# Optimization experiments

Hardware: AMD Instinct MI355X
Metric: run time of the kernel (lower is better)

## Reference

```python
import jax, jax.numpy as jnp
import numpy as np

N, E, M, F, L = 50000, 800000, 50000, 64, 20
HID = 32
NEG_SLOPE = 0.2


def gatv2(x, src, dst, Wl, Wr, att, b, heads, outc):
    # PyG GATv2Conv (eval mode, dropout off), self-loops already in src/dst.
    n = x.shape[0]
    xl = (x @ Wl).reshape(n, heads, outc)
    xr = (x @ Wr).reshape(n, heads, outc)
    e = jax.nn.leaky_relu(xl[src] + xr[dst], NEG_SLOPE)          # [E, H, C]
    score = jnp.einsum('ehc,hc->eh', e, att)                      # [E, H]
    smax = jax.ops.segment_max(score, dst, num_segments=n)
    ex = jnp.exp(score - smax[dst])
    denom = jax.ops.segment_sum(ex, dst, num_segments=n)
    alpha = ex / denom[dst]                                       # scatter-softmax
    out = jax.ops.segment_sum(alpha[:, :, None] * xl[src], dst, num_segments=n)
    return out.reshape(n, heads * outc) + b


def setup_inputs() -> dict:
    key = jax.random.key(0)
    ks = jax.random.split(key, 32)
    d = {}
    d['x'] = jax.random.normal(ks[0], (N, 60), jnp.float32)
    d['lane_x'] = jax.random.normal(ks[1], (M, 2), jnp.float32)
    d['centerline'] = jax.random.normal(ks[2], (F, L, 2), jnp.float32)
    d['edge_index'] = jax.random.randint(ks[3], (2, E), 0, N)
    d['focal_idx'] = jax.random.randint(ks[4], (F,), 0, N)
    s = 0.1
    d['emb_W'] = jax.random.normal(ks[5], (60, HID)) * s
    d['emb_b'] = jnp.zeros((HID,))
    d['c1_Wl'] = jax.random.normal(ks[6], (HID, 4 * HID)) * s
    d['c1_Wr'] = jax.random.normal(ks[7], (HID, 4 * HID)) * s
    d['c1_att'] = jax.random.normal(ks[8], (4, HID)) * s
    d['c1_b'] = jnp.zeros((4 * HID,))
    d['c2_Wl'] = jax.random.normal(ks[9], (4 * HID, 4 * HID)) * s
    d['c2_Wr'] = jax.random.normal(ks[10], (4 * HID, 4 * HID)) * s
    d['c2_att'] = jax.random.normal(ks[11], (4, HID)) * s
    d['c2_b'] = jnp.zeros((4 * HID,))
    d['map_W'] = jax.random.normal(ks[12], (2, HID)) * s
    d['map_b'] = jnp.zeros((HID,))
    d['gg_Wl'] = jax.random.normal(ks[13], (4 * HID, HID)) * s
    d['gg_Wr'] = jax.random.normal(ks[14], (4 * HID, HID)) * s
    d['gg_att'] = jax.random.normal(ks[15], (1, HID)) * s
    d['gg_b'] = jnp.zeros((HID,))
    d['cl_W'] = jax.random.normal(ks[16], (2, HID)) * s
    d['cl_b'] = jnp.zeros((HID,))
    d['fc1_W'] = jax.random.normal(ks[17], (3 * HID, HID)) * s
    d['fc1_b'] = jnp.zeros((HID,))
    d['fc2_W'] = jax.random.normal(ks[18], (HID, HID // 2)) * s
    d['fc2_b'] = jnp.zeros((HID // 2,))
    d['fco_W'] = jax.random.normal(ks[19], (HID // 2, 60)) * s
    d['fco_b'] = jnp.zeros((60,))
    return d


def reference(x, lane_x, centerline, edge_index, focal_idx,
              emb_W, emb_b, c1_Wl, c1_Wr, c1_att, c1_b,
              c2_Wl, c2_Wr, c2_att, c2_b, map_W, map_b,
              gg_Wl, gg_Wr, gg_att, gg_b, cl_W, cl_b,
              fc1_W, fc1_b, fc2_W, fc2_b, fco_W, fco_b):
    n = x.shape[0]
    loops = jnp.arange(n)
    src = jnp.concatenate([edge_index[0], loops])  # PyG adds self-loops
    dst = jnp.concatenate([edge_index[1], loops])
    # agent encoder + subgraph (two GATv2 layers, heads=4, concat)
    h = jax.nn.relu(x @ emb_W + emb_b)                                   # [N,32]
    h = jax.nn.relu(gatv2(h, src, dst, c1_Wl, c1_Wr, c1_att, c1_b, 4, HID))
    agent_feat = jax.nn.relu(gatv2(h, src, dst, c2_Wl, c2_Wr, c2_att, c2_b, 4, HID))  # [N,128]
    # map branch (executable path: no lane edges -> plain embedding + mean pool)
    map_x = jax.nn.relu(lane_x @ map_W + map_b)                          # [M,32]
    map_global = jnp.mean(map_x, axis=0, keepdims=True)                  # [1,32]
    # global graph (heads=1)
    gf = jax.nn.relu(gatv2(agent_feat, src, dst, gg_Wl, gg_Wr, gg_att, gg_b, 1, HID))  # [N,32]
    focal = gf[focal_idx]                                                # [F,32]
    map_g = jnp.broadcast_to(map_global, (focal.shape[0], HID))
    cl = jnp.mean(centerline, axis=1) @ cl_W + cl_b                      # [F,32]
    comb = jnp.concatenate([focal, map_g, cl], axis=1)                   # [F,96]
    h = jax.nn.relu(comb @ fc1_W + fc1_b)
    h = jax.nn.relu(h @ fc2_W + fc2_b)
    return h @ fco_W + fco_b                                             # [F,60]
```

## Files before the change

kernel.cpp:

```cpp
#include <hip/hip_runtime.h>
#include <hip/hip_bf16.h>
#include <hip/hip_fp16.h>

typedef _Float16 half_t;
typedef _Float16 h8 __attribute__((ext_vector_type(8)));
typedef _Float16 h4v __attribute__((ext_vector_type(4)));
typedef _Float16 h2v __attribute__((ext_vector_type(2)));
typedef float f4v __attribute__((ext_vector_type(4)));

static inline int cdiv(long a, long b) { return (int)((a + b - 1) / b); }

__device__ __forceinline__ void fma4(float4& a, float s, const float4& w) {
    a.x += s * w.x; a.y += s * w.y; a.z += s * w.z; a.w += s * w.w;
}


template <int K4, int C4, int R>
__global__ __launch_bounds__(256) void gemm_t_h(
        const float* __restrict__ X, const float* __restrict__ W,
        const float* __restrict__ bias, half_t* __restrict__ Y,
        int Nr, int relu) {
    int idx = blockIdx.x * blockDim.x + threadIdx.x;
    int total = (Nr / R) * C4;
    if (idx >= total) return;
    int c4 = idx % C4;
    int n0 = (idx / C4) * R;
    const float4* __restrict__ Wv = (const float4*)W;
    const float4* __restrict__ Xv = (const float4*)X;
    float4 acc[R];
    float4 binit = bias ? ((const float4*)bias)[c4] : make_float4(0.f, 0.f, 0.f, 0.f);
#pragma unroll
    for (int r = 0; r < R; ++r) acc[r] = binit;
#pragma unroll 4
    for (int k4 = 0; k4 < K4; ++k4) {
        float4 w0 = Wv[(size_t)(4 * k4 + 0) * C4 + c4];
        float4 w1 = Wv[(size_t)(4 * k4 + 1) * C4 + c4];
        float4 w2 = Wv[(size_t)(4 * k4 + 2) * C4 + c4];
        float4 w3 = Wv[(size_t)(4 * k4 + 3) * C4 + c4];
#pragma unroll
        for (int r = 0; r < R; ++r) {
            float4 xv = Xv[(size_t)(n0 + r) * K4 + k4];
            fma4(acc[r], xv.x, w0); fma4(acc[r], xv.y, w1);
            fma4(acc[r], xv.z, w2); fma4(acc[r], xv.w, w3);
        }
    }
#pragma unroll
    for (int r = 0; r < R; ++r) {
        float4 o = acc[r];
        if (relu) {
            o.x = fmaxf(o.x, 0.f); o.y = fmaxf(o.y, 0.f);
            o.z = fmaxf(o.z, 0.f); o.w = fmaxf(o.w, 0.f);
        }
        h4v oh; oh.x = (half_t)o.x; oh.y = (half_t)o.y; oh.z = (half_t)o.z; oh.w = (half_t)o.w;
        ((h4v*)Y)[(size_t)(n0 + r) * C4 + c4] = oh;
    }
}


__global__ void wtrans(const float* __restrict__ c1l, const float* __restrict__ c1r,
                       const float* __restrict__ c2l, const float* __restrict__ c2r,
                       const float* __restrict__ ggl, const float* __restrict__ ggr,
                       half_t* __restrict__ dst) {
    int idx = blockIdx.x * blockDim.x + threadIdx.x;
    if (idx >= 49152) return;
    const float* src; int K, C, loc;
    if (idx < 8192) {
        K = 32; C = 128;
        if (idx < 4096) { src = c1l; loc = idx; } else { src = c1r; loc = idx - 4096; }
    } else if (idx < 40960) {
        K = 128; C = 128;
        if (idx < 24576) { src = c2l; loc = idx - 8192; } else { src = c2r; loc = idx - 24576; }
    } else {
        K = 128; C = 32;
        if (idx < 45056) { src = ggl; loc = idx - 40960; } else { src = ggr; loc = idx - 45056; }
    }
    int k = loc % K, c = loc / K;
    dst[idx] = (half_t)src[k * C + c];
}


template <int K, int C1>
__global__ __launch_bounds__(256) void mfma_dual(
        const half_t* __restrict__ Xh,
        const half_t* __restrict__ W1t, const half_t* __restrict__ W2t,
        half_t* __restrict__ Y1, half_t* __restrict__ Y2, int Nr) {
    constexpr int KT = K / 32;
    constexpr int NBC = (2 * C1) / 64;
    int wave = threadIdx.x >> 6, lane = threadIdx.x & 63;
    int bCol = blockIdx.x % NBC;
    int bRow = blockIdx.x / NBC;
    int rowBase = bRow * 128 + wave * 32;
    int colBase = bCol * 64;
    int m = lane & 15, quad = lane >> 4;

    f4v acc[2][4] = {};

    const half_t* bptr[4];
#pragma unroll
    for (int nt = 0; nt < 4; ++nt) {
        int gc = colBase + nt * 16 + m;
        bptr[nt] = (gc < C1) ? (W1t + (size_t)gc * K) : (W2t + (size_t)(gc - C1) * K);
    }
    int r0 = rowBase + m, r1 = rowBase + 16 + m;
    int r0c = (r0 < Nr) ? r0 : (Nr - 1);
    int r1c = (r1 < Nr) ? r1 : (Nr - 1);
    const half_t* a0p = Xh + (size_t)r0c * K + quad * 8;
    const half_t* a1p = Xh + (size_t)r1c * K + quad * 8;

#pragma unroll
    for (int kk = 0; kk < KT; ++kk) {
        h8 a0 = *(const h8*)(a0p + kk * 32);
        h8 a1 = *(const h8*)(a1p + kk * 32);
#pragma unroll
        for (int nt = 0; nt < 4; ++nt) {
            h8 b = *(const h8*)(bptr[nt] + kk * 32 + quad * 8);
            acc[0][nt] = __builtin_amdgcn_mfma_f32_16x16x32_f16(a0, b, acc[0][nt], 0, 0, 0);
            acc[1][nt] = __builtin_amdgcn_mfma_f32_16x16x32_f16(a1, b, acc[1][nt], 0, 0, 0);
        }
    }

#pragma unroll
    for (int mt = 0; mt < 2; ++mt) {
#pragma unroll
        for (int nt = 0; nt < 4; ++nt) {
            int gc = colBase + nt * 16 + m;
            half_t* Y = (gc < C1) ? (Y1 + gc) : (Y2 + (gc - C1));
#pragma unroll
            for (int r = 0; r < 4; ++r) {
                int gr = rowBase + mt * 16 + quad * 4 + r;
                if (gr < Nr) Y[(size_t)gr * C1] = (half_t)acc[mt][nt][r];
            }
        }
    }
}


__global__ void count_dst(const int* __restrict__ ei, int* __restrict__ counts,
                          int E, int Etot) {
    int e = blockIdx.x * blockDim.x + threadIdx.x;
    if (e >= Etot) return;
    int d = (e < E) ? ei[E + e] : (e - E);
    atomicAdd(&counts[d], 1);
}

#define SCAN_CH 2048

__global__ void reduce_chunks(const int* __restrict__ counts, int* __restrict__ partial, int N) {
    __shared__ int sh[256];
    int t = threadIdx.x, base = blockIdx.x * SCAN_CH + t * 8;
    int s = 0;
    for (int j = 0; j < 8; ++j) if (base + j < N) s += counts[base + j];
    sh[t] = s; __syncthreads();
    for (int off = 128; off >= 1; off >>= 1) {
        if (t < off) sh[t] += sh[t + off];
        __syncthreads();
    }
    if (t == 0) partial[blockIdx.x] = sh[0];
}

__global__ void scan_partials(int* __restrict__ partial, int nch) {
    if (threadIdx.x == 0 && blockIdx.x == 0) {
        int run = 0;
        for (int i = 0; i < nch; ++i) { int v = partial[i]; partial[i] = run; run += v; }
    }
}

__global__ void scan_chunks(const int* __restrict__ counts, const int* __restrict__ partial,
                            int* __restrict__ offsets, int N) {
    __shared__ int sh[256];
    int t = threadIdx.x, b = blockIdx.x, base = b * SCAN_CH + t * 8;
    int v[8], s = 0;
    for (int j = 0; j < 8; ++j) { v[j] = (base + j < N) ? counts[base + j] : 0; s += v[j]; }
    sh[t] = s; __syncthreads();
    for (int off = 1; off < 256; off <<= 1) {
        int x = (t >= off) ? sh[t - off] : 0;
        __syncthreads();
        sh[t] += x;
        __syncthreads();
    }
    int run = partial[b] + (t == 0 ? 0 : sh[t - 1]);
    for (int j = 0; j < 8; ++j) {
        if (base + j < N) offsets[base + j] = run;
        run += v[j];
    }
}

__global__ void fill_adj(const int* __restrict__ ei, const int* __restrict__ offsets,
                         int* __restrict__ cursor, int* __restrict__ adj, int E, int Etot) {
    int e = blockIdx.x * blockDim.x + threadIdx.x;
    if (e >= Etot) return;
    int s, d;
    if (e < E) { s = ei[e]; d = ei[E + e]; } else { s = e - E; d = s; }
    int pos = offsets[d] + atomicAdd(&cursor[d], 1);
    adj[pos] = s;
}


__device__ __forceinline__ float score16h(float x0, float y0, float xrx, float xry, float2 at) {
    float vx = x0 + xrx; vx = (vx > 0.f) ? vx : 0.2f * vx;
    float vy = y0 + xry; vy = (vy > 0.f) ? vy : 0.2f * vy;
    float p = vx * at.x + vy * at.y;
    p += __shfl_xor(p, 1); p += __shfl_xor(p, 2);
    p += __shfl_xor(p, 4); p += __shfl_xor(p, 8);
    return p;
}

__global__ __launch_bounds__(256) void gat_fused_h4_h(
        const half_t* __restrict__ xl, const half_t* __restrict__ xr,
        const float* __restrict__ att, const int* __restrict__ offsets,
        const int* __restrict__ counts, const int* __restrict__ adj,
        const float* __restrict__ bias, half_t* __restrict__ out, int N) {
    int wave = threadIdx.x >> 6, lane = threadIdx.x & 63;
    int d = blockIdx.x * 4 + wave;
    if (d >= N) return;
    int c = lane * 2;
    float2 at = *(const float2*)(att + c);
    h2v xrh = *(const h2v*)(xr + (long)d * 128 + c);
    float xrx = (float)xrh.x, xry = (float)xrh.y;
    int off = offsets[d], deg = counts[d];
    float lsum = 0.f, ax = 0.f, ay = 0.f;
    int i = 0;
    for (; i + 4 <= deg; i += 4) {
        int s0 = adj[off + i + 0], s1 = adj[off + i + 1];
        int s2 = adj[off + i + 2], s3 = adj[off + i + 3];
        h2v h0 = *(const h2v*)(xl + (long)s0 * 128 + c);
        h2v h1 = *(const h2v*)(xl + (long)s1 * 128 + c);
        h2v h2 = *(const h2v*)(xl + (long)s2 * 128 + c);
        h2v h3 = *(const h2v*)(xl + (long)s3 * 128 + c);
        float x0 = (float)h0.x, y0 = (float)h0.y;
        float x1 = (float)h1.x, y1 = (float)h1.y;
        float x2 = (float)h2.x, y2 = (float)h2.y;
        float x3 = (float)h3.x, y3 = (float)h3.y;
        float p0 = score16h(x0, y0, xrx, xry, at);
        float p1 = score16h(x1, y1, xrx, xry, at);
        float p2 = score16h(x2, y2, xrx, xry, at);
        float p3 = score16h(x3, y3, xrx, xry, at);
        float w0 = __expf(p0), w1 = __expf(p1), w2 = __expf(p2), w3 = __expf(p3);
        ax += w0 * x0 + w1 * x1 + w2 * x2 + w3 * x3;
        ay += w0 * y0 + w1 * y1 + w2 * y2 + w3 * y3;
        lsum += (w0 + w1) + (w2 + w3);
    }
    for (; i < deg; ++i) {
        int s = adj[off + i];
        h2v h0 = *(const h2v*)(xl + (long)s * 128 + c);
        float x0 = (float)h0.x, y0 = (float)h0.y;
        float w = __expf(score16h(x0, y0, xrx, xry, at));
        ax += w * x0; ay += w * y0; lsum += w;
    }
    float2 bb = *(const float2*)(bias + c);
    float inv = 1.f / lsum;
    h2v o;
    o.x = (half_t)fmaxf(ax * inv + bb.x, 0.f);
    o.y = (half_t)fmaxf(ay * inv + bb.y, 0.f);
    *(h2v*)(out + (long)d * 128 + c) = o;
}

__device__ __forceinline__ float score32h(float v0, float xr1, float at) {
    float v = v0 + xr1; v = (v > 0.f) ? v : 0.2f * v;
    float p = v * at;
    p += __shfl_xor(p, 1); p += __shfl_xor(p, 2); p += __shfl_xor(p, 4);
    p += __shfl_xor(p, 8); p += __shfl_xor(p, 16);
    return p;
}

__global__ __launch_bounds__(256) void gat_fused_h1_h(
        const half_t* __restrict__ xl, const half_t* __restrict__ xr,
        const float* __restrict__ att, const int* __restrict__ offsets,
        const int* __restrict__ counts, const int* __restrict__ adj,
        const float* __restrict__ bias, float* __restrict__ out, int N) {
    int sub = threadIdx.x >> 5, lane = threadIdx.x & 31;
    int d = blockIdx.x * 8 + sub;
    if (d >= N) return;
    float at = att[lane];
    float xr1 = (float)xr[(long)d * 32 + lane];
    int off = offsets[d], deg = counts[d];
    float lsum = 0.f, acc = 0.f;
    int i = 0;
    for (; i + 4 <= deg; i += 4) {
        int s0 = adj[off + i + 0], s1 = adj[off + i + 1];
        int s2 = adj[off + i + 2], s3 = adj[off + i + 3];
        float x0 = (float)xl[(long)s0 * 32 + lane];
        float x1 = (float)xl[(long)s1 * 32 + lane];
        float x2 = (float)xl[(long)s2 * 32 + lane];
        float x3 = (float)xl[(long)s3 * 32 + lane];
        float w0 = __expf(score32h(x0, xr1, at));
        float w1 = __expf(score32h(x1, xr1, at));
        float w2 = __expf(score32h(x2, xr1, at));
        float w3 = __expf(score32h(x3, xr1, at));
        acc += w0 * x0 + w1 * x1 + w2 * x2 + w3 * x3;
        lsum += (w0 + w1) + (w2 + w3);
    }
    for (; i < deg; ++i) {
        int s = adj[off + i];
        float x0 = (float)xl[(long)s * 32 + lane];
        float w = __expf(score32h(x0, xr1, at));
        acc += w * x0; lsum += w;
    }
    out[(long)d * 32 + lane] = fmaxf(acc / lsum + bias[lane], 0.f);
}


__global__ void map_sum_kernel(const float* __restrict__ lane_x, const float* __restrict__ map_W,
                               const float* __restrict__ map_b, float* __restrict__ sums, int M) {
    __shared__ float s[32];
    if (threadIdx.x < 32) s[threadIdx.x] = 0.f;
    __syncthreads();
    int t = blockIdx.x * blockDim.x + threadIdx.x;
    int nth = gridDim.x * blockDim.x;
    int c = t & 31;
    float w0 = map_W[c], w1 = map_W[32 + c], bb = map_b[c];
    float acc = 0.f;
    for (int m = t >> 5; m < M; m += nth >> 5) {
        float v = lane_x[(long)m * 2] * w0 + lane_x[(long)m * 2 + 1] * w1 + bb;
        acc += fmaxf(v, 0.f);
    }
    atomicAdd(&s[c], acc);
    __syncthreads();
    if (threadIdx.x < 32) atomicAdd(&sums[threadIdx.x], s[threadIdx.x]);
}


__global__ void head_kernel(const float* __restrict__ gf, const int* __restrict__ focal_idx,
                            const float* __restrict__ map_sums, int M,
                            const float* __restrict__ centerline, int L,
                            const float* __restrict__ cl_W, const float* __restrict__ cl_b,
                            const float* __restrict__ fc1_W, const float* __restrict__ fc1_b,
                            const float* __restrict__ fc2_W, const float* __restrict__ fc2_b,
                            const float* __restrict__ fco_W, const float* __restrict__ fco_b,
                            float* __restrict__ out) {
    int f = blockIdx.x;
    int lane = threadIdx.x;
    __shared__ float s_comb[96];
    __shared__ float s_h1[32];
    __shared__ float s_h2[16];
    __shared__ float s_cl[2];

    float c0 = 0.f, c1 = 0.f;
    if (lane < L) {
        c0 = centerline[((long)f * L + lane) * 2 + 0];
        c1 = centerline[((long)f * L + lane) * 2 + 1];
    }
    for (int off = 32; off >= 1; off >>= 1) {
        c0 += __shfl_down(c0, off);
        c1 += __shfl_down(c1, off);
    }
    if (lane == 0) { s_cl[0] = c0 / (float)L; s_cl[1] = c1 / (float)L; }
    __syncthreads();

    int fi = focal_idx[f];
    if (lane < 32) {
        s_comb[lane] = gf[(long)fi * 32 + lane];
        s_comb[32 + lane] = map_sums[lane] / (float)M;
        s_comb[64 + lane] = s_cl[0] * cl_W[lane] + s_cl[1] * cl_W[32 + lane] + cl_b[lane];
    }
    __syncthreads();

    if (lane < 32) {
        float acc = fc1_b[lane];
        for (int k = 0; k < 96; ++k) acc += s_comb[k] * fc1_W[k * 32 + lane];
        s_h1[lane] = fmaxf(acc, 0.f);
    }
    __syncthreads();

    if (lane < 16) {
        float acc = fc2_b[lane];
        for (int k = 0; k < 32; ++k) acc += s_h1[k] * fc2_W[k * 16 + lane];
        s_h2[lane] = fmaxf(acc, 0.f);
    }
    __syncthreads();

    if (lane < 60) {
        float acc = fco_b[lane];
        for (int k = 0; k < 16; ++k) acc += s_h2[k] * fco_W[k * 60 + lane];
        out[(long)f * 60 + lane] = acc;
    }
}


extern "C" void kernel_launch(void* const* d_in, const int* in_sizes, int n_in,
                              void* d_out, int out_size, void* d_ws, size_t ws_size,
                              hipStream_t stream) {
    const float* x          = (const float*)d_in[0];
    const float* lane_x     = (const float*)d_in[1];
    const float* centerline = (const float*)d_in[2];
    const int*   ei         = (const int*)d_in[3];
    const int*   focal_idx  = (const int*)d_in[4];
    const float* emb_W = (const float*)d_in[5];
    const float* emb_b = (const float*)d_in[6];
    const float* c1_Wl = (const float*)d_in[7];
    const float* c1_Wr = (const float*)d_in[8];
    const float* c1_att = (const float*)d_in[9];
    const float* c1_b  = (const float*)d_in[10];
    const float* c2_Wl = (const float*)d_in[11];
    const float* c2_Wr = (const float*)d_in[12];
    const float* c2_att = (const float*)d_in[13];
    const float* c2_b  = (const float*)d_in[14];
    const float* map_W = (const float*)d_in[15];
    const float* map_b = (const float*)d_in[16];
    const float* gg_Wl = (const float*)d_in[17];
    const float* gg_Wr = (const float*)d_in[18];
    const float* gg_att = (const float*)d_in[19];
    const float* gg_b  = (const float*)d_in[20];
    const float* cl_W  = (const float*)d_in[21];
    const float* cl_b  = (const float*)d_in[22];
    const float* fc1_W = (const float*)d_in[23];
    const float* fc1_b = (const float*)d_in[24];
    const float* fc2_W = (const float*)d_in[25];
    const float* fc2_b = (const float*)d_in[26];
    const float* fco_W = (const float*)d_in[27];
    const float* fco_b = (const float*)d_in[28];

    const int N = in_sizes[0] / 60;
    const int M = in_sizes[1] / 2;
    const int F = in_sizes[4];
    const int L = in_sizes[2] / (F * 2);
    const int E = in_sizes[3] / 2;
    const int Etot = E + N;

    half_t* Xl_h = (half_t*)d_ws;
    half_t* Xr_h = Xl_h + (size_t)N * 128;
    half_t* H0_h = Xr_h + (size_t)N * 128;
    half_t* H1_h = H0_h + (size_t)N * 32;
    half_t* AF_h = H1_h + (size_t)N * 128;
    float*  GF_f = (float*)(AF_h + (size_t)N * 128);
    half_t* Wt   = (half_t*)(GF_f + (size_t)N * 32);
    int* counts  = (int*)(Wt + 49152);
    int* offsets = counts + N;
    int* cursor  = offsets + N;
    int* adj     = cursor + N;
    float* MAPS  = (float*)(adj + Etot);
    int* partial = (int*)(MAPS + 32);

    half_t* c1Wlt = Wt + 0;
    half_t* c1Wrt = Wt + 4096;
    half_t* c2Wlt = Wt + 8192;
    half_t* c2Wrt = Wt + 24576;
    half_t* ggWlt = Wt + 40960;
    half_t* ggWrt = Wt + 45056;

    const int BS = 256;
    const int nch = cdiv(N, SCAN_CH);
    const int rowBlocks = cdiv(N, 128);

    hipMemsetAsync(counts, 0, (size_t)N * sizeof(int), stream);
    hipMemsetAsync(cursor, 0, (size_t)N * sizeof(int), stream);
    count_dst<<<cdiv(Etot, BS), BS, 0, stream>>>(ei, counts, E, Etot);
    reduce_chunks<<<nch, 256, 0, stream>>>(counts, partial, N);
    scan_partials<<<1, 64, 0, stream>>>(partial, nch);
    scan_chunks<<<nch, 256, 0, stream>>>(counts, partial, offsets, N);
    fill_adj<<<cdiv(Etot, BS), BS, 0, stream>>>(ei, offsets, cursor, adj, E, Etot);

    wtrans<<<cdiv(49152, BS), BS, 0, stream>>>(c1_Wl, c1_Wr, c2_Wl, c2_Wr, gg_Wl, gg_Wr, Wt);

    gemm_t_h<15, 8, 4><<<cdiv((long)(N / 4) * 8, BS), BS, 0, stream>>>(x, emb_W, emb_b, H0_h, N, 1);

    mfma_dual<32, 128><<<rowBlocks * 4, 256, 0, stream>>>(H0_h, c1Wlt, c1Wrt, Xl_h, Xr_h, N);
    gat_fused_h4_h<<<cdiv(N, 4), 256, 0, stream>>>(Xl_h, Xr_h, c1_att, offsets, counts, adj, c1_b, H1_h, N);

    mfma_dual<128, 128><<<rowBlocks * 4, 256, 0, stream>>>(H1_h, c2Wlt, c2Wrt, Xl_h, Xr_h, N);
    gat_fused_h4_h<<<cdiv(N, 4), 256, 0, stream>>>(Xl_h, Xr_h, c2_att, offsets, counts, adj, c2_b, AF_h, N);

    mfma_dual<128, 32><<<rowBlocks * 1, 256, 0, stream>>>(AF_h, ggWlt, ggWrt, Xl_h, Xr_h, N);
    gat_fused_h1_h<<<cdiv(N, 8), 256, 0, stream>>>(Xl_h, Xr_h, gg_att, offsets, counts, adj, gg_b, GF_f, N);

    hipMemsetAsync(MAPS, 0, 32 * sizeof(float), stream);
    map_sum_kernel<<<64, BS, 0, stream>>>(lane_x, map_W, map_b, MAPS, M);

    head_kernel<<<F, 64, 0, stream>>>(GF_f, focal_idx, MAPS, M, centerline, L,
                                      cl_W, cl_b, fc1_W, fc1_b, fc2_W, fc2_b,
                                      fco_W, fco_b, (float*)d_out);
}
```

Before: 439.2 us.

## Map eight destinations per wave in GAT aggregation with packed fp16 scoring

Rewrites the GATv2 aggregation kernels so each wave handles eight destination nodes with eight lanes each. Each lane loads 16 contiguous fp16 features per neighbor as wide vectors, computes leaky-relu and the attention dot product in packed fp16 (fdot2), and reduces per head with a single shuffle. The aim is to cut shuffle-reduction overhead and raise memory-level parallelism compared with one destination per wave. The cost is that lanes in a wave loop up to the max degree among their eight nodes, leaving some lanes idle. Scores are also now computed in fp16, which loses precision, and the attention vectors are converted to fp16 in the weight-transpose kernel.

```diff
diff --git a/kernel.cpp b/kernel.cpp
--- a/kernel.cpp
+++ b/kernel.cpp
@@ -8,10 +8,42 @@
 typedef _Float16 h2v __attribute__((ext_vector_type(2)));
 typedef float f4v __attribute__((ext_vector_type(4)));
 
+union H8u { h8 v; h2v h2[4]; _Float16 e[8]; };
+union H4u { h4v v; h2v h2[2]; _Float16 e[4]; };
+
 static inline int cdiv(long a, long b) { return (int)((a + b - 1) / b); }
 
 __device__ __forceinline__ void fma4(float4& a, float s, const float4& w) {
     a.x += s * w.x; a.y += s * w.y; a.z += s * w.z; a.w += s * w.w;
+}
+
+__device__ __forceinline__ h8 hmax8(h8 a, h8 b) {
+#if __has_builtin(__builtin_elementwise_max)
+    return __builtin_elementwise_max(a, b);
+#else
+    h8 r;
+#pragma unroll
+    for (int j = 0; j < 8; ++j) r[j] = (a[j] > b[j]) ? a[j] : b[j];
+    return r;
+#endif
+}
+__device__ __forceinline__ h4v hmax4(h4v a, h4v b) {
+#if __has_builtin(__builtin_elementwise_max)
+    return __builtin_elementwise_max(a, b);
+#else
+    h4v r;
+#pragma unroll
+    for (int j = 0; j < 4; ++j) r[j] = (a[j] > b[j]) ? a[j] : b[j];
+    return r;
+#endif
+}
+
+__device__ __forceinline__ float dot2acc(h2v a, h2v b, float c) {
+#if __has_builtin(__builtin_amdgcn_fdot2)
+    return __builtin_amdgcn_fdot2(a, b, c, false);
+#else
+    return c + (float)a.x * (float)b.x + (float)a.y * (float)b.y;
+#endif
 }
 
 
@@ -60,22 +92,33 @@
 __global__ void wtrans(const float* __restrict__ c1l, const float* __restrict__ c1r,
                        const float* __restrict__ c2l, const float* __restrict__ c2r,
                        const float* __restrict__ ggl, const float* __restrict__ ggr,
-                       half_t* __restrict__ dst) {
+                       const float* __restrict__ at1, const float* __restrict__ at2,
+                       const float* __restrict__ atg, half_t* __restrict__ dst) {
     int idx = blockIdx.x * blockDim.x + threadIdx.x;
-    if (idx >= 49152) return;
-    const float* src; int K, C, loc;
+    if (idx >= 49440) return;
+    if (idx >= 49152) {
+        int j = idx - 49152;
+        float v = (j < 128) ? at1[j] : (j < 256) ? at2[j - 128] : atg[j - 256];
+        dst[idx] = (half_t)v;
+        return;
+    }
+    const float* src; int K, loc;
     if (idx < 8192) {
-        K = 32; C = 128;
+        K = 32;
         if (idx < 4096) { src = c1l; loc = idx; } else { src = c1r; loc = idx - 4096; }
+        int k = loc % K, c = loc / K;
+        dst[idx] = (half_t)src[k * 128 + c];
     } else if (idx < 40960) {
-        K = 128; C = 128;
+        K = 128;
         if (idx < 24576) { src = c2l; loc = idx - 8192; } else { src = c2r; loc = idx - 24576; }
+        int k = loc % K, c = loc / K;
+        dst[idx] = (half_t)src[k * 128 + c];
     } else {
-        K = 128; C = 32;
+        K = 128;
         if (idx < 45056) { src = ggl; loc = idx - 40960; } else { src = ggr; loc = idx - 45056; }
-    }
-    int k = loc % K, c = loc / K;
-    dst[idx] = (half_t)src[k * C + c];
+        int k = loc % K, c = loc / K;
+        dst[idx] = (half_t)src[k * 32 + c];
+    }
 }
 
 
@@ -196,107 +239,129 @@
 }
 
 
-__device__ __forceinline__ float score16h(float x0, float y0, float xrx, float xry, float2 at) {
-    float vx = x0 + xrx; vx = (vx > 0.f) ? vx : 0.2f * vx;
-    float vy = y0 + xry; vy = (vy > 0.f) ? vy : 0.2f * vy;
-    float p = vx * at.x + vy * at.y;
-    p += __shfl_xor(p, 1); p += __shfl_xor(p, 2);
-    p += __shfl_xor(p, 4); p += __shfl_xor(p, 8);
-    return p;
-}
-
-__global__ __launch_bounds__(256) void gat_fused_h4_h(
+__global__ __launch_bounds__(256) void gat8_h4(
         const half_t* __restrict__ xl, const half_t* __restrict__ xr,
-        const float* __restrict__ att, const int* __restrict__ offsets,
+        const half_t* __restrict__ atth, const int* __restrict__ offsets,
         const int* __restrict__ counts, const int* __restrict__ adj,
         const float* __restrict__ bias, half_t* __restrict__ out, int N) {
     int wave = threadIdx.x >> 6, lane = threadIdx.x & 63;
-    int d = blockIdx.x * 4 + wave;
-    if (d >= N) return;
-    int c = lane * 2;
-    float2 at = *(const float2*)(att + c);
-    h2v xrh = *(const h2v*)(xr + (long)d * 128 + c);
-    float xrx = (float)xrh.x, xry = (float)xrh.y;
-    int off = offsets[d], deg = counts[d];
-    float lsum = 0.f, ax = 0.f, ay = 0.f;
-    int i = 0;
-    for (; i + 4 <= deg; i += 4) {
-        int s0 = adj[off + i + 0], s1 = adj[off + i + 1];
-        int s2 = adj[off + i + 2], s3 = adj[off + i + 3];
-        h2v h0 = *(const h2v*)(xl + (long)s0 * 128 + c);
-        h2v h1 = *(const h2v*)(xl + (long)s1 * 128 + c);
-        h2v h2 = *(const h2v*)(xl + (long)s2 * 128 + c);
-        h2v h3 = *(const h2v*)(xl + (long)s3 * 128 + c);
-        float x0 = (float)h0.x, y0 = (float)h0.y;
-        float x1 = (float)h1.x, y1 = (float)h1.y;
-        float x2 = (float)h2.x, y2 = (float)h2.y;
-        float x3 = (float)h3.x, y3 = (float)h3.y;
-        float p0 = score16h(x0, y0, xrx, xry, at);
-        float p1 = score16h(x1, y1, xrx, xry, at);
-        float p2 = score16h(x2, y2, xrx, xry, at);
-        float p3 = score16h(x3, y3, xrx, xry, at);
-        float w0 = __expf(p0), w1 = __expf(p1), w2 = __expf(p2), w3 = __expf(p3);
-        ax += w0 * x0 + w1 * x1 + w2 * x2 + w3 * x3;
-        ay += w0 * y0 + w1 * y1 + w2 * y2 + w3 * y3;
-        lsum += (w0 + w1) + (w2 + w3);
-    }
-    for (; i < deg; ++i) {
-        int s = adj[off + i];
-        h2v h0 = *(const h2v*)(xl + (long)s * 128 + c);
-        float x0 = (float)h0.x, y0 = (float)h0.y;
-        float w = __expf(score16h(x0, y0, xrx, xry, at));
-        ax += w * x0; ay += w * y0; lsum += w;
-    }
-    float2 bb = *(const float2*)(bias + c);
-    float inv = 1.f / lsum;
-    h2v o;
-    o.x = (half_t)fmaxf(ax * inv + bb.x, 0.f);
-    o.y = (half_t)fmaxf(ay * inv + bb.y, 0.f);
-    *(h2v*)(out + (long)d * 128 + c) = o;
-}
-
-__device__ __forceinline__ float score32h(float v0, float xr1, float at) {
-    float v = v0 + xr1; v = (v > 0.f) ? v : 0.2f * v;
-    float p = v * at;
-    p += __shfl_xor(p, 1); p += __shfl_xor(p, 2); p += __shfl_xor(p, 4);
-    p += __shfl_xor(p, 8); p += __shfl_xor(p, 16);
-    return p;
-}
-
-__global__ __launch_bounds__(256) void gat_fused_h1_h(
+    int g = lane >> 3, t = lane & 7;
+    int d = blockIdx.x * 32 + wave * 8 + g;
+    int dc = (d < N) ? d : (N - 1);
+    int off = offsets[dc];
+    int deg = (d < N) ? counts[dc] : 0;
+    int dmax = deg;
+    dmax = max(dmax, __shfl_xor(dmax, 8));
+    dmax = max(dmax, __shfl_xor(dmax, 16));
+    dmax = max(dmax, __shfl_xor(dmax, 32));
+
+    const half_t* xrp = xr + (size_t)dc * 128 + t * 16;
+    h8 xr_lo = *(const h8*)(xrp);
+    h8 xr_hi = *(const h8*)(xrp + 8);
+    H8u at_lo, at_hi;
+    at_lo.v = *(const h8*)(atth + t * 16);
+    at_hi.v = *(const h8*)(atth + t * 16 + 8);
+
+    float acc[16];
+#pragma unroll
+    for (int j = 0; j < 16; ++j) acc[j] = 0.f;
+    float lsum = 0.f;
+    h8 c02;
+#pragma unroll
+    for (int j = 0; j < 8; ++j) c02[j] = (half_t)0.2f;
+
+    for (int i = 0; i < dmax; ++i) {
+        bool valid = (i < deg);
+        int s = adj[off + (valid ? i : 0)];
+        const half_t* xp = xl + (size_t)s * 128 + t * 16;
+        H8u a_lo, a_hi;
+        a_lo.v = *(const h8*)(xp);
+        a_hi.v = *(const h8*)(xp + 8);
+        h8 v_lo = a_lo.v + xr_lo;
+        h8 v_hi = a_hi.v + xr_hi;
+        H8u lk_lo, lk_hi;
+        lk_lo.v = hmax8(v_lo, v_lo * c02);
+        lk_hi.v = hmax8(v_hi, v_hi * c02);
+        float p = 0.f;
+#pragma unroll
+        for (int j = 0; j < 4; ++j) p = dot2acc(lk_lo.h2[j], at_lo.h2[j], p);
+#pragma unroll
+        for (int j = 0; j < 4; ++j) p = dot2acc(lk_hi.h2[j], at_hi.h2[j], p);
+        p += __shfl_xor(p, 1);
+        float w = valid ? __expf(p) : 0.f;
+        lsum += w;
+#pragma unroll
+        for (int j = 0; j < 8; ++j) acc[j] += w * (float)a_lo.e[j];
+#pragma unroll
+        for (int j = 0; j < 8; ++j) acc[8 + j] += w * (float)a_hi.e[j];
+    }
+
+    if (d < N) {
+        float inv = 1.f / lsum;
+        H8u o_lo, o_hi;
+#pragma unroll
+        for (int j = 0; j < 8; ++j)
+            o_lo.e[j] = (half_t)fmaxf(acc[j] * inv + bias[t * 16 + j], 0.f);
+#pragma unroll
+        for (int j = 0; j < 8; ++j)
+            o_hi.e[j] = (half_t)fmaxf(acc[8 + j] * inv + bias[t * 16 + 8 + j], 0.f);
+        half_t* op = out + (size_t)d * 128 + t * 16;
+        *(h8*)(op) = o_lo.v;
+        *(h8*)(op + 8) = o_hi.v;
+    }
+}
+
+__global__ __launch_bounds__(256) void gat8_h1(
         const half_t* __restrict__ xl, const half_t* __restrict__ xr,
-        const float* __restrict__ att, const int* __restrict__ offsets,
+        const half_t* __restrict__ atth, const int* __restrict__ offsets,
         const int* __restrict__ counts, const int* __restrict__ adj,
         const float* __restrict__ bias, float* __restrict__ out, int N) {
-    int sub = threadIdx.x >> 5, lane = threadIdx.x & 31;
-    int d = blockIdx.x * 8 + sub;
-    if (d >= N) return;
-    float at = att[lane];
-    float xr1 = (float)xr[(long)d * 32 + lane];
-    int off = offsets[d], deg = counts[d];
-    float lsum = 0.f, acc = 0.f;
-    int i = 0;
-    for (; i + 4 <= deg; i += 4) {
-        int s0 = adj[off + i + 0], s1 = adj[off + i + 1];
-        int s2 = adj[off + i + 2], s3 = adj[off + i + 3];
-        float x0 = (float)xl[(long)s0 * 32 + lane];
-        float x1 = (float)xl[(long)s1 * 32 + lane];
-        float x2 = (float)xl[(long)s2 * 32 + lane];
-        float x3 = (float)xl[(long)s3 * 32 + lane];
-        float w0 = __expf(score32h(x0, xr1, at));
-        float w1 = __expf(score32h(x1, xr1, at));
-        float w2 = __expf(score32h(x2, xr1, at));
-        float w3 = __expf(score32h(x3, xr1, at));
-        acc += w0 * x0 + w1 * x1 + w2 * x2 + w3 * x3;
-        lsum += (w0 + w1) + (w2 + w3);
-    }
-    for (; i < deg; ++i) {
-        int s = adj[off + i];
-        float x0 = (float)xl[(long)s * 32 + lane];
-        float w = __expf(score32h(x0, xr1, at));
-        acc += w * x0; lsum += w;
-    }
-    out[(long)d * 32 + lane] = fmaxf(acc / lsum + bias[lane], 0.f);
+    int wave = threadIdx.x >> 6, lane = threadIdx.x & 63;
+    int g = lane >> 3, t = lane & 7;
+    int d = blockIdx.x * 32 + wave * 8 + g;
+    int dc = (d < N) ? d : (N - 1);
+    int off = offsets[dc];
+    int deg = (d < N) ? counts[dc] : 0;
+    int dmax = deg;
+    dmax = max(dmax, __shfl_xor(dmax, 8));
+    dmax = max(dmax, __shfl_xor(dmax, 16));
+    dmax = max(dmax, __shfl_xor(dmax, 32));
+
+    h4v xr4 = *(const h4v*)(xr + (size_t)dc * 32 + t * 4);
+    H4u at4; at4.v = *(const h4v*)(atth + t * 4);
+
+    float acc[4] = {0.f, 0.f, 0.f, 0.f};
+    float lsum = 0.f;
+    h4v c02;
+#pragma unroll
+    for (int j = 0; j < 4; ++j) c02[j] = (half_t)0.2f;
+
+    for (int i = 0; i < dmax; ++i) {
+        bool valid = (i < deg);
+        int s = adj[off + (valid ? i : 0)];
+        H4u a; a.v = *(const h4v*)(xl + (size_t)s * 32 + t * 4);
+        h4v v = a.v + xr4;
+        H4u lk; lk.v = hmax4(v, v * c02);
+        float p = dot2acc(lk.h2[0], at4.h2[0], 0.f);
+        p = dot2acc(lk.h2[1], at4.h2[1], p);
+        p += __shfl_xor(p, 1);
+        p += __shfl_xor(p, 2);
+        p += __shfl_xor(p, 4);
+        float w = valid ? __expf(p) : 0.f;
+        lsum += w;
+#pragma unroll
+        for (int j = 0; j < 4; ++j) acc[j] += w * (float)a.e[j];
+    }
+
+    if (d < N) {
+        float inv = 1.f / lsum;
+        float4 o;
+        o.x = fmaxf(acc[0] * inv + bias[t * 4 + 0], 0.f);
+        o.y = fmaxf(acc[1] * inv + bias[t * 4 + 1], 0.f);
+        o.z = fmaxf(acc[2] * inv + bias[t * 4 + 2], 0.f);
+        o.w = fmaxf(acc[3] * inv + bias[t * 4 + 3], 0.f);
+        *(float4*)(out + (size_t)d * 32 + t * 4) = o;
+    }
 }
 
 
@@ -424,7 +489,7 @@
     half_t* AF_h = H1_h + (size_t)N * 128;
     float*  GF_f = (float*)(AF_h + (size_t)N * 128);
     half_t* Wt   = (half_t*)(GF_f + (size_t)N * 32);
-    int* counts  = (int*)(Wt + 49152);
+    int* counts  = (int*)(Wt + 49440);
     int* offsets = counts + N;
     int* cursor  = offsets + N;
     int* adj     = cursor + N;
@@ -437,6 +502,9 @@
     half_t* c2Wrt = Wt + 24576;
     half_t* ggWlt = Wt + 40960;
     half_t* ggWrt = Wt + 45056;
+    half_t* att1h = Wt + 49152;
+    half_t* att2h = Wt + 49280;
+    half_t* attgh = Wt + 49408;
 
     const int BS = 256;
     const int nch = cdiv(N, SCAN_CH);
@@ -450,18 +518,19 @@
     scan_chunks<<<nch, 256, 0, stream>>>(counts, partial, offsets, N);
     fill_adj<<<cdiv(Etot, BS), BS, 0, stream>>>(ei, offsets, cursor, adj, E, Etot);
 
-    wtrans<<<cdiv(49152, BS), BS, 0, stream>>>(c1_Wl, c1_Wr, c2_Wl, c2_Wr, gg_Wl, gg_Wr, Wt);
+    wtrans<<<cdiv(49440, BS), BS, 0, stream>>>(c1_Wl, c1_Wr, c2_Wl, c2_Wr, gg_Wl, gg_Wr,
+                                               c1_att, c2_att, gg_att, Wt);
 
     gemm_t_h<15, 8, 4><<<cdiv((long)(N / 4) * 8, BS), BS, 0, stream>>>(x, emb_W, emb_b, H0_h, N, 1);
 
     mfma_dual<32, 128><<<rowBlocks * 4, 256, 0, stream>>>(H0_h, c1Wlt, c1Wrt, Xl_h, Xr_h, N);
-    gat_fused_h4_h<<<cdiv(N, 4), 256, 0, stream>>>(Xl_h, Xr_h, c1_att, offsets, counts, adj, c1_b, H1_h, N);
+    gat8_h4<<<cdiv(N, 32), 256, 0, stream>>>(Xl_h, Xr_h, att1h, offsets, counts, adj, c1_b, H1_h, N);
 
     mfma_dual<128, 128><<<rowBlocks * 4, 256, 0, stream>>>(H1_h, c2Wlt, c2Wrt, Xl_h, Xr_h, N);
-    gat_fused_h4_h<<<cdiv(N, 4), 256, 0, stream>>>(Xl_h, Xr_h, c2_att, offsets, counts, adj, c2_b, AF_h, N);
+    gat8_h4<<<cdiv(N, 32), 256, 0, stream>>>(Xl_h, Xr_h, att2h, offsets, counts, adj, c2_b, AF_h, N);
 
     mfma_dual<128, 32><<<rowBlocks * 1, 256, 0, stream>>>(AF_h, ggWlt, ggWrt, Xl_h, Xr_h, N);
-    gat_fused_h1_h<<<cdiv(N, 8), 256, 0, stream>>>(Xl_h, Xr_h, gg_att, offsets, counts, adj, gg_b, GF_f, N);
+    gat8_h1<<<cdiv(N, 32), 256, 0, stream>>>(Xl_h, Xr_h, attgh, offsets, counts, adj, gg_b, GF_f, N);
 
     hipMemsetAsync(MAPS, 0, 32 * sizeof(float), stream);
     map_sum_kernel<<<64, BS, 0, stream>>>(lane_x, map_W, map_b, MAPS, M);
```

Result: faster. 397.8 us (-9.4%).
